# Kernel optimization log

Measured on AMD Instinct MI355X. Metric: run time of the kernel, lower is better.

## Reference

```python
import jax, jax.numpy as jnp
import numpy as np

SIZE = 8192      # codebook entries
CODE_DIM = 256   # code vector dim


def setup_inputs() -> dict:
    key = jax.random.key(0)
    k1, k2 = jax.random.split(key)
    z = jax.random.normal(k1, (16, CODE_DIM, 32, 32), dtype=jnp.float32)
    # nn.Embedding weight initialized uniform(-1/size, 1/size)
    emb = jax.random.uniform(k2, (SIZE, CODE_DIM), dtype=jnp.float32,
                             minval=-1.0 / SIZE, maxval=1.0 / SIZE)
    return {"z": z, "emb": emb}


def reference(z, emb):
    n, c, h, w = z.shape
    # [N, C, H, W] -> [N*H*W, C]
    z_ = jnp.transpose(z, (0, 2, 3, 1)).reshape(-1, c)
    # squared euclidean distances, expanded form: ||z||^2 - 2 z.e + ||e||^2
    distances = ((z_ * z_).sum(axis=1, keepdims=True)
                 - 2.0 * jnp.matmul(z_, emb.T)
                 + (emb * emb).sum(axis=1)[None, :])  # [N*H*W, SIZE]
    encoding_indices = jnp.argmin(distances, axis=1).reshape(n, h, w)
    # gather + back to NCHW
    quantized = jnp.transpose(emb[encoding_indices], (0, 3, 1, 2))
    # straight-through estimator: value == quantized, grad flows to z
    st = z + jax.lax.stop_gradient(quantized - z)
    return quantized, st, encoding_indices
```

## Files before the change

### kernel.cpp

```cpp
#include <hip/hip_runtime.h>
#include <float.h>


typedef int i32x4  __attribute__((ext_vector_type(4)));
typedef int i32x16 __attribute__((ext_vector_type(16)));

#define KDIM 256
#define NCODES 8192
#define MTOTAL 16384
#define MT 64
#define ST_OFF 4194304
#define IDX_OFF 8388608
#define MARGIN 2.5e-4f
#define CANDCAP 1024
#define SEINV (8192.0f * 127.0f)
#define SE2 (2.0f / (8192.0f * 127.0f))

__device__ __forceinline__ int swz_idx(int row, int k) {
    return (row << 8) + ((((k >> 2) ^ ((row >> 2) & 7)) << 2) | (k & 3));
}
__device__ __forceinline__ unsigned quant4(float4 v, float inv) {
    const int a = (int)rintf(v.x * inv), b = (int)rintf(v.y * inv);
    const int c = (int)rintf(v.z * inv), d = (int)rintf(v.w * inv);
    return (a & 255) | ((b & 255) << 8) | ((c & 255) << 16) | ((unsigned)(d & 255) << 24);
}

__global__ void emb_pack(const float* __restrict__ emb, unsigned* __restrict__ ws) {
    __shared__ unsigned lq[32 * 65];
    const int grp = blockIdx.x, t = threadIdx.x;
    const float4* base = (const float4*)(emb + (size_t)grp * 32 * KDIM);
    #pragma unroll
    for (int i = 0; i < 8; ++i) {
        const int f = i * 256 + t;
        lq[(f >> 6) * 65 + (f & 63)] = quant4(base[f], SEINV);
    }
    __syncthreads();
    uint4* wq = (uint4*)ws + (size_t)grp * 512;
    #pragma unroll
    for (int u = 0; u < 2; ++u) {
        const int F = u * 256 + t;
        const int ch = F >> 6, lane = F & 63;
        const unsigned* s = lq + (lane & 31) * 65 + 8 * ch + 2 * (lane >> 5);
        uint4 o; o.x = s[0]; o.y = s[1]; o.z = s[4]; o.w = s[5];
        wq[F] = o;
    }
}

__global__ __launch_bounds__(512, 2) void vq_mfma(
    const float* __restrict__ z, const float* __restrict__ emb,
    const unsigned* __restrict__ ebf, float* __restrict__ out)
{
    __shared__ float  zT[MT * KDIM];
    __shared__ double z2part[MT][8];
    __shared__ float  zmaxp[MT][8];
    __shared__ float  z2s[MT];
    __shared__ float  szs[MT];
    __shared__ float  red_d[MT * 16 * 4];
    __shared__ int    red_n[MT * 16 * 4];
    __shared__ float  best_s[MT];
    __shared__ int    bestn_s[MT];
    __shared__ unsigned long long packed_s[MT];
    __shared__ int    cand[CANDCAP];
    __shared__ int    candcnt;
    __shared__ int    idx_s[MT];

    const int tid  = threadIdx.x;
    const int lane = tid & 63;
    const int W    = tid >> 6;
    const int m0   = blockIdx.x * MT;
    const int nimg = m0 >> 10;
    const int hw0  = m0 & 1023;

    {
        const float* zb = z + (size_t)nimg * (KDIM * 1024) + hw0 + lane;
        const int ks = W * 32;
        #pragma unroll 8
        for (int i = 0; i < 32; ++i) {
            const int k = ks + i;
            zT[swz_idx(lane, k)] = zb[(size_t)k * 1024];
        }
    }
    if (tid == 0) candcnt = 0;
    __syncthreads();

    {
        const int row = tid >> 3, ks = (tid & 7) << 5;
        double s = 0.0; float mx = 0.f;
        for (int k = ks; k < ks + 32; ++k) {
            const float v = zT[swz_idx(row, k)];
            s = fma((double)v, (double)v, s);
            mx = fmaxf(mx, fabsf(v));
        }
        z2part[row][tid & 7] = s;
        zmaxp[row][tid & 7] = mx;
    }
    __syncthreads();
    if (tid < MT) {
        double s = 0.0; float mx = 1e-30f;
        #pragma unroll
        for (int p = 0; p < 8; ++p) { s += z2part[tid][p]; mx = fmaxf(mx, zmaxp[tid][p]); }
        z2s[tid] = (float)s;
        szs[tid] = mx / 127.0f;
        packed_s[tid] = ~0ull;
    }
    __syncthreads();

    const int r0 = lane & 31, r1 = 32 + r0;
    const int p  = lane >> 5;
    i32x4 zq0[8], zq1[8];
    {
        const float inv0 = 1.0f / szs[r0];
        const float inv1 = 1.0f / szs[r1];
        const int key0 = (r0 >> 2) & 7, key1 = (r1 >> 2) & 7;
        const float* zr0 = zT + (r0 << 8);
        const float* zr1 = zT + (r1 << 8);
        #pragma unroll
        for (int t = 0; t < 8; ++t) {
            const int q0 = 8 * t + 2 * p;
            i32x4 a, b;
            a[0] = (int)quant4(*(const float4*)(zr0 + (((q0 + 0) ^ key0) << 2)), inv0);
            a[1] = (int)quant4(*(const float4*)(zr0 + (((q0 + 1) ^ key0) << 2)), inv0);
            a[2] = (int)quant4(*(const float4*)(zr0 + (((q0 + 4) ^ key0) << 2)), inv0);
            a[3] = (int)quant4(*(const float4*)(zr0 + (((q0 + 5) ^ key0) << 2)), inv0);
            zq0[t] = a;
            b[0] = (int)quant4(*(const float4*)(zr1 + (((q0 + 0) ^ key1) << 2)), inv1);
            b[1] = (int)quant4(*(const float4*)(zr1 + (((q0 + 1) ^ key1) << 2)), inv1);
            b[2] = (int)quant4(*(const float4*)(zr1 + (((q0 + 4) ^ key1) << 2)), inv1);
            b[3] = (int)quant4(*(const float4*)(zr1 + (((q0 + 5) ^ key1) << 2)), inv1);
            zq1[t] = b;
        }
    }

    float s1a = -FLT_MAX, s2a = -FLT_MAX, s3a = -FLT_MAX, s4a = -FLT_MAX;
    float s1b = -FLT_MAX, s2b = -FLT_MAX, s3b = -FLT_MAX, s4b = -FLT_MAX;
    {
        const i32x4* ap0 = (const i32x4*)ebf + ((size_t)W * 32 * 512 + lane);
        i32x4 pfA[8], pfB[8];
        #pragma unroll
        for (int t = 0; t < 8; ++t) pfA[t] = ap0[t * 64];
        #pragma unroll
        for (int t = 0; t < 8; ++t) pfB[t] = ap0[512 + t * 64];

        for (int gl = 0; gl < 32; gl += 2) {
            #pragma unroll
            for (int par = 0; par < 2; ++par) {
                const int g = gl + par;
                i32x16 acc0, acc1;
                #pragma unroll
                for (int i = 0; i < 16; ++i) { acc0[i] = 0; acc1[i] = 0; }

                __builtin_amdgcn_s_setprio(1);
                if (par == 0) {
                    #pragma unroll
                    for (int t = 0; t < 8; ++t) {
                        acc0 = __builtin_amdgcn_mfma_i32_32x32x32_i8(pfA[t], zq0[t], acc0, 0, 0, 0);
                        acc1 = __builtin_amdgcn_mfma_i32_32x32x32_i8(pfA[t], zq1[t], acc1, 0, 0, 0);
                    }
                } else {
                    #pragma unroll
                    for (int t = 0; t < 8; ++t) {
                        acc0 = __builtin_amdgcn_mfma_i32_32x32x32_i8(pfB[t], zq0[t], acc0, 0, 0, 0);
                        acc1 = __builtin_amdgcn_mfma_i32_32x32x32_i8(pfB[t], zq1[t], acc1, 0, 0, 0);
                    }
                }
                __builtin_amdgcn_s_setprio(0);

                {
                    const i32x4* apn = ap0 + (size_t)((g + 2) & 31) * 512;
                    if (par == 0) {
                        #pragma unroll
                        for (int t = 0; t < 8; ++t) pfA[t] = apn[t * 64];
                    } else {
                        #pragma unroll
                        for (int t = 0; t < 8; ++t) pfB[t] = apn[t * 64];
                    }
                }

                const unsigned gtag = (unsigned)(g << 4);
                #pragma unroll
                for (int r = 0; r < 16; ++r) {
                    {
                        const float kf = (float)acc0[r];
                        const float kk = __uint_as_float(
                            (__float_as_uint(kf) & 0xFFFFFE00u) | (gtag | (unsigned)r));
                        const float o1 = s1a, o2 = s2a, o3 = s3a, o4 = s4a;
                        s1a = fmaxf(kk, o1);
                        s2a = fmaxf(fminf(kk, o1), o2);
                        s3a = fmaxf(fminf(kk, o2), o3);
                        s4a = fmaxf(fminf(kk, o3), o4);
                    }
                    {
                        const float kf = (float)acc1[r];
                        const float kk = __uint_as_float(
                            (__float_as_uint(kf) & 0xFFFFFE00u) | (gtag | (unsigned)r));
                        const float o1 = s1b, o2 = s2b, o3 = s3b, o4 = s4b;
                        s1b = fmaxf(kk, o1);
                        s2b = fmaxf(fminf(kk, o1), o2);
                        s3b = fmaxf(fminf(kk, o2), o3);
                        s4b = fmaxf(fminf(kk, o3), o4);
                    }
                }
            }
        }
    }

    {
        const float z2r0 = z2s[r0], z2r1 = z2s[r1];
        const float c0 = SE2 * szs[r0], c1 = SE2 * szs[r1];
        const int L = (W << 1) | p;
        const int b0 = (r0 * 16 + L) * 4, b1i = (r1 * 16 + L) * 4;
        const int cw = W * 1024 + 4 * p;
        float sa[4] = {s1a, s2a, s3a, s4a};
        float sb[4] = {s1b, s2b, s3b, s4b};
        #pragma unroll
        for (int s = 0; s < 4; ++s) {
            const unsigned ua = __float_as_uint(sa[s]);
            const unsigned gg = (ua >> 4) & 31, rr = ua & 15;
            red_d[b0 + s] = z2r0 - c0 * sa[s];
            red_n[b0 + s] = cw + (int)(gg * 32 + (rr & 3) + ((rr >> 2) << 3));
            const unsigned ub = __float_as_uint(sb[s]);
            const unsigned gg2 = (ub >> 4) & 31, rr2 = ub & 15;
            red_d[b1i + s] = z2r1 - c1 * sb[s];
            red_n[b1i + s] = cw + (int)(gg2 * 32 + (rr2 & 3) + ((rr2 >> 2) << 3));
        }
    }
    __syncthreads();

    if (tid < MT) {
        float B1 = FLT_MAX, B2 = FLT_MAX;
        int   N1 = 0x7FFFFFFF;
        for (int t = 0; t < 16; ++t) {
            const int base = (tid * 16 + t) * 4;
            const float c1 = red_d[base + 0]; const int cn = red_n[base + 0];
            const float c2 = red_d[base + 1];
            if (c1 < B1 || (c1 == B1 && cn < N1)) { B2 = fminf(B1, c2); B1 = c1; N1 = cn; }
            else B2 = fminf(B2, c1);
        }
        best_s[tid] = B1; bestn_s[tid] = N1;
        if (B2 - B1 <= MARGIN) {
            const float thr = B1 + MARGIN;
            for (int t = 0; t < 16; ++t) {
                const int base = (tid * 16 + t) * 4;
                #pragma unroll
                for (int s = 0; s < 4; ++s) {
                    if (red_d[base + s] <= thr) {
                        const int pos = atomicAdd(&candcnt, 1);
                        if (pos < CANDCAP) cand[pos] = (tid << 16) | red_n[base + s];
                    }
                }
            }
        }
    }
    __syncthreads();

    {
        const int C = min(candcnt, CANDCAP);
        for (int c = tid; c < C; c += 512) {
            const int rw = cand[c] >> 16, n = cand[c] & 0xFFFF;
            const float4* er = (const float4*)(emb + (size_t)n * KDIM);
            const int key = (rw >> 2) & 7;
            const float* zr = zT + (rw << 8);
            double dd = 0.0;
            for (int kq = 0; kq < 64; ++kq) {
                const float4 ev = er[kq];
                const float4 zv = *(const float4*)(zr + ((kq ^ key) << 2));
                dd = fma((double)zv.x, (double)ev.x, dd);
                dd = fma((double)zv.y, (double)ev.y, dd);
                dd = fma((double)zv.z, (double)ev.z, dd);
                dd = fma((double)zv.w, (double)ev.w, dd);
            }
            const float dg = z2s[rw] - 2.f * (float)dd;
            const unsigned long long keyp =
                ((unsigned long long)__float_as_uint(dg) << 32)
                | (unsigned long long)(unsigned)n;
            atomicMin(&packed_s[rw], keyp);
        }
    }
    __syncthreads();

    if (tid < MT) {
        int n = bestn_s[tid];
        if (packed_s[tid] != ~0ull) n = (int)(packed_s[tid] & 0xFFFFFFFFull);
        idx_s[tid] = n;
        out[IDX_OFF + m0 + tid] = (float)n;
    }
    __syncthreads();

    {
        const int rr = tid & 15;
        const int cb = tid >> 4;
        const int i0 = idx_s[4 * rr + 0], i1 = idx_s[4 * rr + 1];
        const int i2 = idx_s[4 * rr + 2], i3 = idx_s[4 * rr + 3];
        const size_t ob = (size_t)nimg * 262144 + hw0 + 4 * rr;
        for (int c = cb; c < KDIM; c += 32) {
            float4 qv;
            qv.x = emb[(size_t)i0 * KDIM + c];
            qv.y = emb[(size_t)i1 * KDIM + c];
            qv.z = emb[(size_t)i2 * KDIM + c];
            qv.w = emb[(size_t)i3 * KDIM + c];
            *(float4*)(out + ob + (size_t)c * 1024) = qv;
            *(float4*)(out + ST_OFF + ob + (size_t)c * 1024) = qv;
        }
    }
}

extern "C" void kernel_launch(void* const* d_in, const int* in_sizes, int n_in,
                              void* d_out, int out_size, void* d_ws, size_t ws_size,
                              hipStream_t stream) {
    const float* zp   = (const float*)d_in[0];
    const float* embp = (const float*)d_in[1];
    float* outp = (float*)d_out;
    unsigned* ws = (unsigned*)d_ws;
    emb_pack<<<NCODES / 32, 256, 0, stream>>>(embp, ws);
    vq_mfma<<<MTOTAL / MT, 512, 0, stream>>>(zp, embp, ws, outp);
}
```

Baseline: 153.2 us.

## Halve row tile to 32, use integer top-3 tracking, raise occupancy to 4 blocks

Halves the rows per block from 64 to 32, so each wave keeps one quantized z fragment and one accumulator instead of two. It also drops the double-buffered codebook prefetch and replaces the float-based top-4 tracking with an integer top-3 that packs the index tag into the low bits. Launch bounds now ask for 4 blocks per CU to raise occupancy. The cost is that codebook fragments are reused across half as many rows, so L2 traffic for the codebook doubles, and keeping one fewer candidate per lane may send more rows to the exact-rescore path.

```diff
diff --git a/kernel.cpp b/kernel.cpp
--- a/kernel.cpp
+++ b/kernel.cpp
@@ -8,11 +8,11 @@
 #define KDIM 256
 #define NCODES 8192
 #define MTOTAL 16384
-#define MT 64
+#define MT 32
 #define ST_OFF 4194304
 #define IDX_OFF 8388608
 #define MARGIN 2.5e-4f
-#define CANDCAP 1024
+#define CANDCAP 512
 #define SEINV (8192.0f * 127.0f)
 #define SE2 (2.0f / (8192.0f * 127.0f))
 
@@ -46,17 +46,17 @@
     }
 }
 
-__global__ __launch_bounds__(512, 2) void vq_mfma(
+__global__ __launch_bounds__(512, 4) void vq_mfma(
     const float* __restrict__ z, const float* __restrict__ emb,
     const unsigned* __restrict__ ebf, float* __restrict__ out)
 {
     __shared__ float  zT[MT * KDIM];
-    __shared__ double z2part[MT][8];
-    __shared__ float  zmaxp[MT][8];
+    __shared__ double z2part[MT][16];
+    __shared__ float  zmaxp[MT][16];
     __shared__ float  z2s[MT];
     __shared__ float  szs[MT];
-    __shared__ float  red_d[MT * 16 * 4];
-    __shared__ int    red_n[MT * 16 * 4];
+    __shared__ float  red_d[MT * 16 * 3];
+    __shared__ int    red_n[MT * 16 * 3];
     __shared__ float  best_s[MT];
     __shared__ int    bestn_s[MT];
     __shared__ unsigned long long packed_s[MT];
@@ -72,156 +72,107 @@
     const int hw0  = m0 & 1023;
 
     {
-        const float* zb = z + (size_t)nimg * (KDIM * 1024) + hw0 + lane;
-        const int ks = W * 32;
+        const int row = tid & 31, kc = tid >> 5;
+        const float* zb = z + (size_t)nimg * (KDIM * 1024) + hw0 + row;
         #pragma unroll 8
-        for (int i = 0; i < 32; ++i) {
-            const int k = ks + i;
-            zT[swz_idx(lane, k)] = zb[(size_t)k * 1024];
+        for (int i = 0; i < 16; ++i) {
+            const int k = kc * 16 + i;
+            zT[swz_idx(row, k)] = zb[(size_t)k * 1024];
         }
     }
     if (tid == 0) candcnt = 0;
     __syncthreads();
 
     {
-        const int row = tid >> 3, ks = (tid & 7) << 5;
+        const int row = tid >> 4, ks = (tid & 15) << 4;
         double s = 0.0; float mx = 0.f;
-        for (int k = ks; k < ks + 32; ++k) {
+        for (int k = ks; k < ks + 16; ++k) {
             const float v = zT[swz_idx(row, k)];
             s = fma((double)v, (double)v, s);
             mx = fmaxf(mx, fabsf(v));
         }
-        z2part[row][tid & 7] = s;
-        zmaxp[row][tid & 7] = mx;
+        z2part[row][tid & 15] = s;
+        zmaxp[row][tid & 15] = mx;
     }
     __syncthreads();
     if (tid < MT) {
         double s = 0.0; float mx = 1e-30f;
         #pragma unroll
-        for (int p = 0; p < 8; ++p) { s += z2part[tid][p]; mx = fmaxf(mx, zmaxp[tid][p]); }
+        for (int p = 0; p < 16; ++p) { s += z2part[tid][p]; mx = fmaxf(mx, zmaxp[tid][p]); }
         z2s[tid] = (float)s;
         szs[tid] = mx / 127.0f;
         packed_s[tid] = ~0ull;
     }
     __syncthreads();
 
-    const int r0 = lane & 31, r1 = 32 + r0;
+    const int r  = lane & 31;
     const int p  = lane >> 5;
-    i32x4 zq0[8], zq1[8];
-    {
-        const float inv0 = 1.0f / szs[r0];
-        const float inv1 = 1.0f / szs[r1];
-        const int key0 = (r0 >> 2) & 7, key1 = (r1 >> 2) & 7;
-        const float* zr0 = zT + (r0 << 8);
-        const float* zr1 = zT + (r1 << 8);
+    i32x4 zq[8];
+    {
+        const float inv = 1.0f / szs[r];
+        const int key = (r >> 2) & 7;
+        const float* zr = zT + (r << 8);
         #pragma unroll
         for (int t = 0; t < 8; ++t) {
             const int q0 = 8 * t + 2 * p;
-            i32x4 a, b;
-            a[0] = (int)quant4(*(const float4*)(zr0 + (((q0 + 0) ^ key0) << 2)), inv0);
-            a[1] = (int)quant4(*(const float4*)(zr0 + (((q0 + 1) ^ key0) << 2)), inv0);
-            a[2] = (int)quant4(*(const float4*)(zr0 + (((q0 + 4) ^ key0) << 2)), inv0);
-            a[3] = (int)quant4(*(const float4*)(zr0 + (((q0 + 5) ^ key0) << 2)), inv0);
-            zq0[t] = a;
-            b[0] = (int)quant4(*(const float4*)(zr1 + (((q0 + 0) ^ key1) << 2)), inv1);
-            b[1] = (int)quant4(*(const float4*)(zr1 + (((q0 + 1) ^ key1) << 2)), inv1);
-            b[2] = (int)quant4(*(const float4*)(zr1 + (((q0 + 4) ^ key1) << 2)), inv1);
-            b[3] = (int)quant4(*(const float4*)(zr1 + (((q0 + 5) ^ key1) << 2)), inv1);
-            zq1[t] = b;
-        }
-    }
-
-    float s1a = -FLT_MAX, s2a = -FLT_MAX, s3a = -FLT_MAX, s4a = -FLT_MAX;
-    float s1b = -FLT_MAX, s2b = -FLT_MAX, s3b = -FLT_MAX, s4b = -FLT_MAX;
+            i32x4 a;
+            a[0] = (int)quant4(*(const float4*)(zr + (((q0 + 0) ^ key) << 2)), inv);
+            a[1] = (int)quant4(*(const float4*)(zr + (((q0 + 1) ^ key) << 2)), inv);
+            a[2] = (int)quant4(*(const float4*)(zr + (((q0 + 4) ^ key) << 2)), inv);
+            a[3] = (int)quant4(*(const float4*)(zr + (((q0 + 5) ^ key) << 2)), inv);
+            zq[t] = a;
+        }
+    }
+
+    int s1 = 0x80000000, s2 = 0x80000000, s3 = 0x80000000;
     {
         const i32x4* ap0 = (const i32x4*)ebf + ((size_t)W * 32 * 512 + lane);
-        i32x4 pfA[8], pfB[8];
-        #pragma unroll
-        for (int t = 0; t < 8; ++t) pfA[t] = ap0[t * 64];
-        #pragma unroll
-        for (int t = 0; t < 8; ++t) pfB[t] = ap0[512 + t * 64];
-
-        for (int gl = 0; gl < 32; gl += 2) {
+        i32x4 pf[8];
+        #pragma unroll
+        for (int t = 0; t < 8; ++t) pf[t] = ap0[t * 64];
+
+        for (int g = 0; g < 32; ++g) {
+            i32x16 acc;
             #pragma unroll
-            for (int par = 0; par < 2; ++par) {
-                const int g = gl + par;
-                i32x16 acc0, acc1;
+            for (int i = 0; i < 16; ++i) acc[i] = 0;
+
+            __builtin_amdgcn_s_setprio(1);
+            #pragma unroll
+            for (int t = 0; t < 8; ++t)
+                acc = __builtin_amdgcn_mfma_i32_32x32x32_i8(pf[t], zq[t], acc, 0, 0, 0);
+            __builtin_amdgcn_s_setprio(0);
+
+            {
+                const i32x4* apn = ap0 + (size_t)((g + 1) & 31) * 512;
                 #pragma unroll
-                for (int i = 0; i < 16; ++i) { acc0[i] = 0; acc1[i] = 0; }
-
-                __builtin_amdgcn_s_setprio(1);
-                if (par == 0) {
-                    #pragma unroll
-                    for (int t = 0; t < 8; ++t) {
-                        acc0 = __builtin_amdgcn_mfma_i32_32x32x32_i8(pfA[t], zq0[t], acc0, 0, 0, 0);
-                        acc1 = __builtin_amdgcn_mfma_i32_32x32x32_i8(pfA[t], zq1[t], acc1, 0, 0, 0);
-                    }
-                } else {
-                    #pragma unroll
-                    for (int t = 0; t < 8; ++t) {
-                        acc0 = __builtin_amdgcn_mfma_i32_32x32x32_i8(pfB[t], zq0[t], acc0, 0, 0, 0);
-                        acc1 = __builtin_amdgcn_mfma_i32_32x32x32_i8(pfB[t], zq1[t], acc1, 0, 0, 0);
-                    }
-                }
-                __builtin_amdgcn_s_setprio(0);
-
-                {
-                    const i32x4* apn = ap0 + (size_t)((g + 2) & 31) * 512;
-                    if (par == 0) {
-                        #pragma unroll
-                        for (int t = 0; t < 8; ++t) pfA[t] = apn[t * 64];
-                    } else {
-                        #pragma unroll
-                        for (int t = 0; t < 8; ++t) pfB[t] = apn[t * 64];
-                    }
-                }
-
-                const unsigned gtag = (unsigned)(g << 4);
-                #pragma unroll
-                for (int r = 0; r < 16; ++r) {
-                    {
-                        const float kf = (float)acc0[r];
-                        const float kk = __uint_as_float(
-                            (__float_as_uint(kf) & 0xFFFFFE00u) | (gtag | (unsigned)r));
-                        const float o1 = s1a, o2 = s2a, o3 = s3a, o4 = s4a;
-                        s1a = fmaxf(kk, o1);
-                        s2a = fmaxf(fminf(kk, o1), o2);
-                        s3a = fmaxf(fminf(kk, o2), o3);
-                        s4a = fmaxf(fminf(kk, o3), o4);
-                    }
-                    {
-                        const float kf = (float)acc1[r];
-                        const float kk = __uint_as_float(
-                            (__float_as_uint(kf) & 0xFFFFFE00u) | (gtag | (unsigned)r));
-                        const float o1 = s1b, o2 = s2b, o3 = s3b, o4 = s4b;
-                        s1b = fmaxf(kk, o1);
-                        s2b = fmaxf(fminf(kk, o1), o2);
-                        s3b = fmaxf(fminf(kk, o2), o3);
-                        s4b = fmaxf(fminf(kk, o3), o4);
-                    }
-                }
-            }
-        }
-    }
-
-    {
-        const float z2r0 = z2s[r0], z2r1 = z2s[r1];
-        const float c0 = SE2 * szs[r0], c1 = SE2 * szs[r1];
+                for (int t = 0; t < 8; ++t) pf[t] = apn[t * 64];
+            }
+
+            const int gtag = g << 4;
+            #pragma unroll
+            for (int rr = 0; rr < 16; ++rr) {
+                const int kk = (acc[rr] << 9) | (gtag | rr);
+                const int t1 = min(kk, s1); s1 = max(kk, s1);
+                const int t2 = min(t1, s2); s2 = max(t1, s2);
+                s3 = max(t2, s3);
+            }
+        }
+    }
+
+    {
+        const float z2r = z2s[r];
+        const float c0  = SE2 * szs[r];
         const int L = (W << 1) | p;
-        const int b0 = (r0 * 16 + L) * 4, b1i = (r1 * 16 + L) * 4;
+        const int b0 = (r * 16 + L) * 3;
         const int cw = W * 1024 + 4 * p;
-        float sa[4] = {s1a, s2a, s3a, s4a};
-        float sb[4] = {s1b, s2b, s3b, s4b};
-        #pragma unroll
-        for (int s = 0; s < 4; ++s) {
-            const unsigned ua = __float_as_uint(sa[s]);
-            const unsigned gg = (ua >> 4) & 31, rr = ua & 15;
-            red_d[b0 + s] = z2r0 - c0 * sa[s];
+        int sk[3] = {s1, s2, s3};
+        #pragma unroll
+        for (int s = 0; s < 3; ++s) {
+            const int idot = sk[s] >> 9;
+            const unsigned tag = (unsigned)sk[s] & 511u;
+            const unsigned gg = tag >> 4, rr = tag & 15;
+            red_d[b0 + s] = z2r - c0 * (float)idot;
             red_n[b0 + s] = cw + (int)(gg * 32 + (rr & 3) + ((rr >> 2) << 3));
-            const unsigned ub = __float_as_uint(sb[s]);
-            const unsigned gg2 = (ub >> 4) & 31, rr2 = ub & 15;
-            red_d[b1i + s] = z2r1 - c1 * sb[s];
-            red_n[b1i + s] = cw + (int)(gg2 * 32 + (rr2 & 3) + ((rr2 >> 2) << 3));
         }
     }
     __syncthreads();
@@ -230,7 +181,7 @@
         float B1 = FLT_MAX, B2 = FLT_MAX;
         int   N1 = 0x7FFFFFFF;
         for (int t = 0; t < 16; ++t) {
-            const int base = (tid * 16 + t) * 4;
+            const int base = (tid * 16 + t) * 3;
             const float c1 = red_d[base + 0]; const int cn = red_n[base + 0];
             const float c2 = red_d[base + 1];
             if (c1 < B1 || (c1 == B1 && cn < N1)) { B2 = fminf(B1, c2); B1 = c1; N1 = cn; }
@@ -240,9 +191,9 @@
         if (B2 - B1 <= MARGIN) {
             const float thr = B1 + MARGIN;
             for (int t = 0; t < 16; ++t) {
-                const int base = (tid * 16 + t) * 4;
+                const int base = (tid * 16 + t) * 3;
                 #pragma unroll
-                for (int s = 0; s < 4; ++s) {
+                for (int s = 0; s < 3; ++s) {
                     if (red_d[base + s] <= thr) {
                         const int pos = atomicAdd(&candcnt, 1);
                         if (pos < CANDCAP) cand[pos] = (tid << 16) | red_n[base + s];
@@ -287,12 +238,12 @@
     __syncthreads();
 
     {
-        const int rr = tid & 15;
-        const int cb = tid >> 4;
-        const int i0 = idx_s[4 * rr + 0], i1 = idx_s[4 * rr + 1];
-        const int i2 = idx_s[4 * rr + 2], i3 = idx_s[4 * rr + 3];
-        const size_t ob = (size_t)nimg * 262144 + hw0 + 4 * rr;
-        for (int c = cb; c < KDIM; c += 32) {
+        const int rg = tid & 7;
+        const int cb = tid >> 3;
+        const int i0 = idx_s[4 * rg + 0], i1 = idx_s[4 * rg + 1];
+        const int i2 = idx_s[4 * rg + 2], i3 = idx_s[4 * rg + 3];
+        const size_t ob = (size_t)nimg * 262144 + hw0 + 4 * rg;
+        for (int c = cb; c < KDIM; c += 64) {
             float4 qv;
             qv.x = emb[(size_t)i0 * KDIM + c];
             qv.y = emb[(size_t)i1 * KDIM + c];
```

Measured after the change: 145.3 us. -5.1%, faster.
